# Performance work log

Hardware: AMD Instinct MI355X
Metric: run time of the kernel (lower is better)

The kernel has to match this reference:

```python
import jax, jax.numpy as jnp
import numpy as np

N, E, F = 50000, 1600000, 128
H1, C1 = 8, 16   # conv1: heads=8, out=16 -> concat 128
H2, C2 = 1, 16   # conv2: heads=1, out=num_classes=16


def _gat_conv(x, edge_index, W, a_src, a_dst, b, heads, out_ch):
    """PyG GATConv with self-loops, additive attention, dst-segmented softmax."""
    n = x.shape[0]
    loop = jnp.arange(n, dtype=edge_index.dtype)
    src = jnp.concatenate([edge_index[0], loop])  # [Et]
    dst = jnp.concatenate([edge_index[1], loop])  # [Et]
    h = (x @ W).reshape(n, heads, out_ch)                      # [N,H,C]
    alpha_s = jnp.sum(h * a_src[None], axis=-1)                # [N,H]
    alpha_d = jnp.sum(h * a_dst[None], axis=-1)                # [N,H]
    e = jax.nn.leaky_relu(alpha_s[src] + alpha_d[dst], 0.2)    # [Et,H]
    # segment softmax over destination node (self-loops guarantee nonempty segments)
    m = jax.lax.stop_gradient(jax.ops.segment_max(e, dst, num_segments=n))
    ex = jnp.exp(e - m[dst])
    denom = jax.ops.segment_sum(ex, dst, num_segments=n)
    alpha = ex / denom[dst]                                    # [Et,H]
    msg = h[src] * alpha[:, :, None]                           # [Et,H,C]
    out = jax.ops.segment_sum(msg, dst, num_segments=n)        # [N,H,C]
    return out.reshape(n, heads * out_ch) + b


def setup_inputs() -> dict:
    key = jax.random.key(0)
    ks = jax.random.split(key, 10)
    sc = 0.1
    x = jax.random.normal(ks[0], (N, F), dtype=jnp.float32)
    edge_index = jax.random.randint(ks[1], (2, E), 0, N, dtype=jnp.int32)
    return {
        "x": x,
        "edge_index": edge_index,
        "W1": jax.random.normal(ks[2], (F, H1 * C1), dtype=jnp.float32) * sc,
        "a_src1": jax.random.normal(ks[3], (H1, C1), dtype=jnp.float32) * sc,
        "a_dst1": jax.random.normal(ks[4], (H1, C1), dtype=jnp.float32) * sc,
        "b1": jnp.zeros((H1 * C1,), dtype=jnp.float32),
        "W2": jax.random.normal(ks[5], (H1 * C1, H2 * C2), dtype=jnp.float32) * sc,
        "a_src2": jax.random.normal(ks[6], (H2, C2), dtype=jnp.float32) * sc,
        "a_dst2": jax.random.normal(ks[7], (H2, C2), dtype=jnp.float32) * sc,
        "b2": jnp.zeros((H2 * C2,), dtype=jnp.float32),
    }


def reference(x, edge_index, W1, a_src1, a_dst1, b1, W2, a_src2, a_dst2, b2):
    h = _gat_conv(x, edge_index, W1, a_src1, a_dst1, b1, H1, C1)
    h = jax.nn.elu(h)
    # dropout p=0.6 is identity in eval mode
    return _gat_conv(h, edge_index, W2, a_src2, a_dst2, b2, H2, C2)
```

## Files before the change

kernel.cpp:

```cpp
#include <hip/hip_runtime.h>
#include <hip/hip_bf16.h>

#define NN 50000
#define NE 1600000
#define ET (NE + NN)
#define H1 8
#define C1 16
#define D1 128
#define C2 16
#define NB1 196
#define OCTW 6250
#define NSL 64
#define SLE (NE / NSL)

#define HIST_NB 512
#define PACK_NB 1563
#define SCAT_NB 512
#define GEMM_NB 782

typedef unsigned short u16;
typedef unsigned int u32;
typedef u32 u32x4 __attribute__((ext_vector_type(4)));

__device__ void hist_role(int hbid, char* smem, const int* __restrict__ ei,
                          u16* __restrict__ hs) {
  int* hl = (int*)smem;
  const int oct = hbid & 7;
  const int s   = hbid >> 3;
  const int lo  = oct * OCTW;
  const int tid = threadIdx.x;
  for (int j = tid; j < OCTW; j += 256) hl[j] = 0;
  __syncthreads();
  const int4* dp = (const int4*)(ei + NE) + (size_t)s * (SLE / 4);
  for (int g = tid; g < SLE / 4; g += 256) {
    int4 v = dp[g];
    int a = v.x - lo, b = v.y - lo, c = v.z - lo, d = v.w - lo;
    if ((unsigned)a < OCTW) atomicAdd(&hl[a], 1);
    if ((unsigned)b < OCTW) atomicAdd(&hl[b], 1);
    if ((unsigned)c < OCTW) atomicAdd(&hl[c], 1);
    if ((unsigned)d < OCTW) atomicAdd(&hl[d], 1);
  }
  __syncthreads();
  u16* out = hs + (size_t)s * NN + lo;
  for (int j = tid; j < OCTW; j += 256) out[j] = (u16)hl[j];
}

__device__ void pack_role(int pbid, const int* __restrict__ ei,
                          u16* __restrict__ src16, u16* __restrict__ dst16) {
  int i = pbid * 256 + threadIdx.x;
  if (i >= NE / 4) return;
  int4 s = ((const int4*)ei)[i];
  int4 d = ((const int4*)(ei + NE))[i];
  ushort4 sp; sp.x = (u16)s.x; sp.y = (u16)s.y; sp.z = (u16)s.z; sp.w = (u16)s.w;
  ushort4 dp; dp.x = (u16)d.x; dp.y = (u16)d.y; dp.z = (u16)d.z; dp.w = (u16)d.w;
  ((ushort4*)src16)[i] = sp;
  ((ushort4*)dst16)[i] = dp;
}

__global__ __launch_bounds__(256) void k1_fused(const int* __restrict__ ei,
    u16* __restrict__ hs, u16* __restrict__ src16, u16* __restrict__ dst16) {
  __shared__ __align__(16) char smem[25088];
  const int bid = blockIdx.x;
  if (bid < HIST_NB) hist_role(bid, smem, ei, hs);
  else pack_role(bid - HIST_NB, ei, src16, dst16);
}

__global__ __launch_bounds__(256) void scan1_k(u16* __restrict__ hs,
                                               int* __restrict__ deg32,
                                               int* __restrict__ incl,
                                               int* __restrict__ bsum) {
  __shared__ int sm[256];
  int t = threadIdx.x, i = blockIdx.x * 256 + t;
  int v = 0;
  if (i < NN) {
    int run = 0;
#pragma unroll
    for (int s = 0; s < NSL; ++s) {
      int c = (int)hs[(size_t)s * NN + i];
      hs[(size_t)s * NN + i] = (u16)run;
      run += c;
    }
    v = run + 1;
    deg32[i] = v;
  }
  sm[t] = v; __syncthreads();
  for (int off = 1; off < 256; off <<= 1) {
    int u = (t >= off) ? sm[t - off] : 0;
    __syncthreads();
    sm[t] += u;
    __syncthreads();
  }
  if (i < NN) incl[i] = sm[t];
  if (t == 255) bsum[blockIdx.x] = sm[255];
}

__global__ __launch_bounds__(256) void scan2_k(const int* __restrict__ bsum, int* __restrict__ boff) {
  __shared__ int sm[256];
  int t = threadIdx.x;
  int v = (t < NB1) ? bsum[t] : 0;
  sm[t] = v; __syncthreads();
  for (int off = 1; off < 256; off <<= 1) {
    int u = (t >= off) ? sm[t - off] : 0;
    __syncthreads();
    sm[t] += u;
    __syncthreads();
  }
  if (t < NB1) boff[t] = sm[t] - v;
}

__global__ __launch_bounds__(256) void scan3_k(const int* __restrict__ deg32,
                                               const int* __restrict__ incl,
                                               const int* __restrict__ boff,
                                               int* __restrict__ rowptr,
                                               u16* __restrict__ srcs) {
  int i = blockIdx.x * 256 + threadIdx.x;
  if (i >= NN) return;
  int dg = deg32[i];
  int r = incl[i] - dg + boff[i >> 8];
  rowptr[i] = r;
  srcs[r + dg - 1] = (u16)i;
  if (i == 0) rowptr[NN] = ET;
}

__device__ void scatter_role(int sbid, char* smem, const u16* __restrict__ src16,
    const u16* __restrict__ dst16, const int* __restrict__ rowptr,
    const u16* __restrict__ hs, u16* __restrict__ srcs) {
  int* cur = (int*)smem;
  const int oct = sbid & 7;
  const int s   = sbid >> 3;
  const int lo  = oct * OCTW;
  const int tid = threadIdx.x;
  const u16* seed = hs + (size_t)s * NN + lo;
  for (int j = tid; j < OCTW; j += 256)
    cur[j] = rowptr[lo + j] + (int)seed[j];
  __syncthreads();
  const u32x4* dp = (const u32x4*)dst16 + (size_t)s * (SLE / 8);
  const u32x4* sp = (const u32x4*)src16 + (size_t)s * (SLE / 8);
  for (int g = tid; g < SLE / 8; g += 256) {
    u32x4 dv = __builtin_nontemporal_load(&dp[g]);
    u32x4 sv = __builtin_nontemporal_load(&sp[g]);
#pragma unroll
    for (int q = 0; q < 4; ++q) {
      int d0 = (int)(dv[q] & 0xffffu) - lo;
      int d1 = (int)(dv[q] >> 16) - lo;
      if ((unsigned)d0 < OCTW) srcs[atomicAdd(&cur[d0], 1)] = (u16)(sv[q] & 0xffffu);
      if ((unsigned)d1 < OCTW) srcs[atomicAdd(&cur[d1], 1)] = (u16)(sv[q] >> 16);
    }
  }
}

__device__ void gemm1_role(int bid, char* smem, const float* __restrict__ X,
    const float* __restrict__ W, const float* __restrict__ aS,
    const float* __restrict__ aD, __hip_bfloat16* __restrict__ Yb,
    float* __restrict__ as1, float* __restrict__ ad1) {
  float (*Xs)[68]  = (float(*)[68])smem;
  float (*Wt)[128] = (float(*)[128])(smem + 8704);
  const int tid = threadIdx.x;
  const int tx = tid & 31;
  const int ty = tid >> 5;
  const int row0 = bid * 64;
  float acc[8][4] = {};

  for (int kt = 0; kt < D1; kt += 32) {
    {
      int r = tid >> 3, c4 = tid & 7;
#pragma unroll
      for (int it = 0; it < 2; ++it) {
        int row = r + it * 32;
        int grow = row0 + row; if (grow > NN - 1) grow = NN - 1;
        float4 v = *(const float4*)(X + (size_t)grow * D1 + kt + c4 * 4);
        Xs[c4 * 4 + 0][row] = v.x; Xs[c4 * 4 + 1][row] = v.y;
        Xs[c4 * 4 + 2][row] = v.z; Xs[c4 * 4 + 3][row] = v.w;
      }
    }
#pragma unroll
    for (int it = 0; it < 4; ++it) {
      int idx = it * 256 + tid;
      int kk = idx >> 5, cc = (idx & 31) * 4;
      *(float4*)&Wt[kk][cc] = *(const float4*)(W + (size_t)(kt + kk) * D1 + cc);
    }
    __syncthreads();
#pragma unroll
    for (int k = 0; k < 32; ++k) {
      float4 w4 = *(const float4*)&Wt[k][tx * 4];
      float4 xa = *(const float4*)&Xs[k][ty * 8];
      float4 xb = *(const float4*)&Xs[k][ty * 8 + 4];
      float xv[8] = {xa.x, xa.y, xa.z, xa.w, xb.x, xb.y, xb.z, xb.w};
      float wv[4] = {w4.x, w4.y, w4.z, w4.w};
#pragma unroll
      for (int rr = 0; rr < 8; ++rr)
#pragma unroll
        for (int cc = 0; cc < 4; ++cc)
          acc[rr][cc] = fmaf(xv[rr], wv[cc], acc[rr][cc]);
    }
    __syncthreads();
  }

  const int h = tx >> 2;
  const int cin = (tx * 4) & 15;
  float a_sv[4], a_dv[4];
#pragma unroll
  for (int j = 0; j < 4; ++j) { a_sv[j] = aS[h * 16 + cin + j]; a_dv[j] = aD[h * 16 + cin + j]; }
#pragma unroll
  for (int rr = 0; rr < 8; ++rr) {
    int grow = row0 + ty * 8 + rr;
    if (grow < NN) {
      union { ushort4 u; __hip_bfloat16 hh[4]; } pk;
      pk.hh[0] = __float2bfloat16(acc[rr][0]);
      pk.hh[1] = __float2bfloat16(acc[rr][1]);
      pk.hh[2] = __float2bfloat16(acc[rr][2]);
      pk.hh[3] = __float2bfloat16(acc[rr][3]);
      *(ushort4*)(Yb + (size_t)grow * D1 + tx * 4) = pk.u;
      float ps = acc[rr][0] * a_sv[0] + acc[rr][1] * a_sv[1] + acc[rr][2] * a_sv[2] + acc[rr][3] * a_sv[3];
      float pd = acc[rr][0] * a_dv[0] + acc[rr][1] * a_dv[1] + acc[rr][2] * a_dv[2] + acc[rr][3] * a_dv[3];
      ps += __shfl_xor(ps, 1); pd += __shfl_xor(pd, 1);
      ps += __shfl_xor(ps, 2); pd += __shfl_xor(pd, 2);
      if ((tx & 3) == 0) { as1[grow * H1 + h] = ps; ad1[grow * H1 + h] = pd; }
    }
  }
}

__global__ __launch_bounds__(256) void k2_fused(const u16* __restrict__ src16,
    const u16* __restrict__ dst16, const int* __restrict__ rowptr,
    const u16* __restrict__ hs, u16* __restrict__ srcs,
    const float* __restrict__ X, const float* __restrict__ W,
    const float* __restrict__ aS, const float* __restrict__ aD,
    __hip_bfloat16* __restrict__ Yb, float* __restrict__ as1, float* __restrict__ ad1) {
  __shared__ __align__(16) char smem[25088];
  const int bid = blockIdx.x;
  if (bid < SCAT_NB) scatter_role(bid, smem, src16, dst16, rowptr, hs, srcs);
  else gemm1_role(bid - SCAT_NB, smem, X, W, aS, aD, Yb, as1, ad1);
}

__global__ __launch_bounds__(128) void agg1_k(const int* __restrict__ rowptr,
    const u16* __restrict__ srcs, const u32* __restrict__ h1u,
    const float* __restrict__ as, const float* __restrict__ ad,
    const float* __restrict__ b, float* __restrict__ z) {
  __shared__ int ssrc[2][64];
  __shared__ float wl[2][64 * 9];
  __shared__ int lens[2];
  const int w = threadIdx.x >> 6;
  const int lane = threadIdx.x & 63;
  const int d = blockIdx.x * 2 + w;
  const int h = lane >> 3;
  const int beg = rowptr[d], end = rowptr[d + 1];
  if (lane == 0) lens[w] = end - beg;
  __syncthreads();
  const int nb = (max(lens[0], lens[1]) + 63) >> 6;
  const float4 adv0 = *(const float4*)(ad + (size_t)d * H1);
  const float4 adv1 = *(const float4*)(ad + (size_t)d * H1 + 4);
  float aL0 = 0, aL1 = 0, aL2 = 0, aL3 = 0;
  float aH0 = 0, aH1 = 0, aH2 = 0, aH3 = 0;
  float dn0 = 0, dn1 = 0, dn2 = 0, dn3 = 0;
  for (int it = 0; it < nb; ++it) {
    const int base = beg + (it << 6);
    int m = end - base; m = m < 0 ? 0 : (m > 64 ? 64 : m);
    if (lane < m) {
      int s = (int)srcs[base + lane];
      ssrc[w][lane] = s;
      const float4 a0 = *(const float4*)(as + (size_t)s * H1);
      const float4 a1 = *(const float4*)(as + (size_t)s * H1 + 4);
      float* wp = &wl[w][lane * 9];
      float e;
      e = a0.x + adv0.x; e = e > 0.f ? e : 0.2f * e; wp[0] = __expf(e);
      e = a0.y + adv0.y; e = e > 0.f ? e : 0.2f * e; wp[1] = __expf(e);
      e = a0.z + adv0.z; e = e > 0.f ? e : 0.2f * e; wp[2] = __expf(e);
      e = a0.w + adv0.w; e = e > 0.f ? e : 0.2f * e; wp[3] = __expf(e);
      e = a1.x + adv1.x; e = e > 0.f ? e : 0.2f * e; wp[4] = __expf(e);
      e = a1.y + adv1.y; e = e > 0.f ? e : 0.2f * e; wp[5] = __expf(e);
      e = a1.z + adv1.z; e = e > 0.f ? e : 0.2f * e; wp[6] = __expf(e);
      e = a1.w + adv1.w; e = e > 0.f ? e : 0.2f * e; wp[7] = __expf(e);
    }
    __syncthreads();
    int j = 0;
    for (; j + 4 <= m; j += 4) {
      int s0 = ssrc[w][j], s1 = ssrc[w][j + 1], s2 = ssrc[w][j + 2], s3 = ssrc[w][j + 3];
      float w0 = wl[w][(j + 0) * 9 + h], w1 = wl[w][(j + 1) * 9 + h];
      float w2 = wl[w][(j + 2) * 9 + h], w3 = wl[w][(j + 3) * 9 + h];
      u32 v0 = h1u[(size_t)s0 * 64 + lane];
      u32 v1 = h1u[(size_t)s1 * 64 + lane];
      u32 v2 = h1u[(size_t)s2 * 64 + lane];
      u32 v3 = h1u[(size_t)s3 * 64 + lane];
      dn0 += w0; dn1 += w1; dn2 += w2; dn3 += w3;
      aL0 = fmaf(w0, __uint_as_float(v0 << 16), aL0);
      aH0 = fmaf(w0, __uint_as_float(v0 & 0xffff0000u), aH0);
      aL1 = fmaf(w1, __uint_as_float(v1 << 16), aL1);
      aH1 = fmaf(w1, __uint_as_float(v1 & 0xffff0000u), aH1);
      aL2 = fmaf(w2, __uint_as_float(v2 << 16), aL2);
      aH2 = fmaf(w2, __uint_as_float(v2 & 0xffff0000u), aH2);
      aL3 = fmaf(w3, __uint_as_float(v3 << 16), aL3);
      aH3 = fmaf(w3, __uint_as_float(v3 & 0xffff0000u), aH3);
    }
    for (; j < m; ++j) {
      int s0 = ssrc[w][j];
      float w0 = wl[w][j * 9 + h];
      u32 v0 = h1u[(size_t)s0 * 64 + lane];
      dn0 += w0;
      aL0 = fmaf(w0, __uint_as_float(v0 << 16), aL0);
      aH0 = fmaf(w0, __uint_as_float(v0 & 0xffff0000u), aH0);
    }
    __syncthreads();
  }
  float den = (dn0 + dn1) + (dn2 + dn3);
  float aL = (aL0 + aL1) + (aL2 + aL3);
  float aH = (aH0 + aH1) + (aH2 + aH3);
  float inv = 1.f / den;
  float2 bb = *(const float2*)(b + lane * 2);
  float v0 = aL * inv + bb.x;
  float v1 = aH * inv + bb.y;
  v0 = v0 > 0.f ? v0 : __expf(v0) - 1.f;
  v1 = v1 > 0.f ? v1 : __expf(v1) - 1.f;
  float2 o = {v0, v1};
  *(float2*)(z + (size_t)d * D1 + lane * 2) = o;
}

__global__ __launch_bounds__(256) void gemm2_k(const float* __restrict__ Z,
    const float* __restrict__ W, const float* __restrict__ aS,
    const float* __restrict__ aD, __hip_bfloat16* __restrict__ Yb,
    float* __restrict__ as2, float* __restrict__ ad2) {
  __shared__ float Ws[D1][C2];
  __shared__ float Zs[16][D1 + 4];
  const int tid = threadIdx.x;
  for (int i = tid; i < D1 * C2; i += 256) Ws[i >> 4][i & 15] = W[i];
  const int rb = blockIdx.x * 16;
  {
    int r = tid >> 5, c4 = (tid & 31) * 4;
#pragma unroll
    for (int it = 0; it < 2; ++it) {
      int rr = r + it * 8;
      float4 v = *(const float4*)(Z + (size_t)(rb + rr) * D1 + c4);
      *(float4*)&Zs[rr][c4] = v;
    }
  }
  __syncthreads();
  const int r = tid >> 4, c = tid & 15;
  float a0 = 0, a1 = 0, a2 = 0, a3 = 0;
#pragma unroll
  for (int k = 0; k < D1; k += 4) {
    float4 z4 = *(const float4*)&Zs[r][k];
    a0 = fmaf(z4.x, Ws[k][c], a0);
    a1 = fmaf(z4.y, Ws[k + 1][c], a1);
    a2 = fmaf(z4.z, Ws[k + 2][c], a2);
    a3 = fmaf(z4.w, Ws[k + 3][c], a3);
  }
  float acc = (a0 + a1) + (a2 + a3);
  Yb[(size_t)(rb + r) * C2 + c] = __float2bfloat16(acc);
  float ps = acc * aS[c], pd = acc * aD[c];
  ps += __shfl_xor(ps, 1); pd += __shfl_xor(pd, 1);
  ps += __shfl_xor(ps, 2); pd += __shfl_xor(pd, 2);
  ps += __shfl_xor(ps, 4); pd += __shfl_xor(pd, 4);
  ps += __shfl_xor(ps, 8); pd += __shfl_xor(pd, 8);
  if (c == 0) { as2[rb + r] = ps; ad2[rb + r] = pd; }
}

__global__ __launch_bounds__(256) void agg2_k(const int* __restrict__ rowptr,
    const u16* __restrict__ srcs, const u32* __restrict__ h2u,
    const float* __restrict__ as, const float* __restrict__ ad,
    const float* __restrict__ b, float* __restrict__ outp) {
  const int wv = threadIdx.x >> 6;
  const int lane = threadIdx.x & 63;
  const int d = blockIdx.x * 4 + wv;
  const int j8 = lane >> 3, cp = lane & 7;
  const int beg = rowptr[d], end = rowptr[d + 1];
  const float adv = ad[d];
  float a0 = 0, a1 = 0, den = 0;
  for (int base = beg; base < end; base += 64) {
    const int m = end - base;
    float wreg = 0.f; int sreg = 0;
    if (lane < m) {
      sreg = (int)srcs[base + lane];
      float e = as[sreg] + adv;
      e = e > 0.f ? e : 0.2f * e;
      wreg = __expf(e);
    }
    const int mm = m < 64 ? m : 64;
    const int rounds = (mm + 7) >> 3;
    for (int r = 0; r < rounds; ++r) {
      int src_lane = r * 8 + j8;
      float wgt = __shfl(wreg, src_lane);
      int s     = __shfl(sreg, src_lane);
      if (wgt > 0.f) {
        u32 v = h2u[(size_t)s * 8 + cp];
        den += wgt;
        a0 = fmaf(wgt, __uint_as_float(v << 16), a0);
        a1 = fmaf(wgt, __uint_as_float(v & 0xffff0000u), a1);
      }
    }
  }
#pragma unroll
  for (int off = 8; off < 64; off <<= 1) {
    a0 += __shfl_xor(a0, off);
    a1 += __shfl_xor(a1, off);
    den += __shfl_xor(den, off);
  }
  if (j8 == 0) {
    float inv = 1.f / den;
    float2 bb = *(const float2*)(b + cp * 2);
    float2 o = {a0 * inv + bb.x, a1 * inv + bb.y};
    *(float2*)(outp + (size_t)d * C2 + cp * 2) = o;
  }
}

extern "C" void kernel_launch(void* const* d_in, const int* in_sizes, int n_in,
                              void* d_out, int out_size, void* d_ws, size_t ws_size,
                              hipStream_t stream) {
  const float* x    = (const float*)d_in[0];
  const int*   ei   = (const int*)d_in[1];
  const float* W1   = (const float*)d_in[2];
  const float* aS1  = (const float*)d_in[3];
  const float* aD1  = (const float*)d_in[4];
  const float* b1   = (const float*)d_in[5];
  const float* W2   = (const float*)d_in[6];
  const float* aS2  = (const float*)d_in[7];
  const float* aD2  = (const float*)d_in[8];
  const float* b2   = (const float*)d_in[9];
  float* outp = (float*)d_out;

  char* p = (char*)d_ws;
  __hip_bfloat16* h1b = (__hip_bfloat16*)p; p += (size_t)NN * D1 * 2;
  float* z    = (float*)p; p += (size_t)NN * D1 * 4;
  float* as1  = (float*)p; p += (size_t)NN * H1 * 4;
  float* ad1  = (float*)p; p += (size_t)NN * H1 * 4;
  u16*   hs     = (u16*)p; p += (size_t)NSL * NN * 2;
  int*   deg32  = (int*)p; p += (size_t)NN * 4;
  int*   incl   = (int*)p; p += (size_t)NN * 4;
  int*   rowptr = (int*)p; p += (size_t)(NN + 1) * 4;
  int*   bsum   = (int*)p; p += 256 * 4;
  int*   boff   = (int*)p; p += 256 * 4;
  u16*   srcs   = (u16*)p; p += (size_t)ET * 2;
  u16*   src16  = (u16*)p; p += (size_t)NE * 2;
  u16*   dst16  = (u16*)p; p += (size_t)NE * 2;
  __hip_bfloat16* h2b = h1b;
  float* as2 = (float*)(h1b + (size_t)NN * C2);
  float* ad2 = as2 + NN;

  k1_fused<<<HIST_NB + PACK_NB, 256, 0, stream>>>(ei, hs, src16, dst16);

  scan1_k<<<NB1, 256, 0, stream>>>(hs, deg32, incl, bsum);
  scan2_k<<<1, 256, 0, stream>>>(bsum, boff);
  scan3_k<<<NB1, 256, 0, stream>>>(deg32, incl, boff, rowptr, srcs);

  k2_fused<<<SCAT_NB + GEMM_NB, 256, 0, stream>>>(
      src16, dst16, rowptr, hs, srcs, x, W1, aS1, aD1, h1b, as1, ad1);

  agg1_k <<<NN / 2, 128, 0, stream>>>(rowptr, srcs, (const u32*)h1b, as1, ad1, b1, z);

  gemm2_k<<<NN / 16, 256, 0, stream>>>(z, W2, aS2, aD2, h2b, as2, ad2);
  agg2_k <<<NN / 4, 256, 0, stream>>>(rowptr, srcs, (const u32*)h2b, as2, ad2, b2, outp);
}
```

Baseline: 253.7 us.

## Use bf16 MFMA for layer-1 GEMM with folded attention weights, store z as bf16

Adds a small prep role that transposes W1 to bf16 and appends folded attention vectors W1·a_src and W1·a_dst as extra output columns. The layer-1 GEMM then runs on MFMA 16x16x32 bf16 instructions and produces the attention logits in the same pass. The fp32 scalar-FMA tiling and the separate reduction are removed. The layer-1 output z is also stored as bf16, which halves its write and read traffic in gemm2. The cost is lower precision in x, the folded attention logits and z, which could hurt accuracy.

```diff
diff --git a/kernel.cpp b/kernel.cpp
--- a/kernel.cpp
+++ b/kernel.cpp
@@ -15,12 +15,15 @@
 
 #define HIST_NB 512
 #define PACK_NB 1563
+#define PREP_NB 8
 #define SCAT_NB 512
 #define GEMM_NB 782
 
 typedef unsigned short u16;
 typedef unsigned int u32;
 typedef u32 u32x4 __attribute__((ext_vector_type(4)));
+typedef __bf16 bf16x8 __attribute__((ext_vector_type(8)));
+typedef float f32x4v __attribute__((ext_vector_type(4)));
 
 __device__ void hist_role(int hbid, char* smem, const int* __restrict__ ei,
                           u16* __restrict__ hs) {
@@ -57,12 +60,37 @@
   ((ushort4*)dst16)[i] = dp;
 }
 
+__device__ void prep_role(int pbid, const float* __restrict__ W1,
+    const float* __restrict__ aS, const float* __restrict__ aD,
+    __hip_bfloat16* __restrict__ WextT) {
+  const int k = threadIdx.x;
+  if (k >= 128) return;
+  const int h = pbid;
+#pragma unroll
+  for (int j = 0; j < 16; ++j) {
+    int n = h * 16 + j;
+    WextT[(size_t)n * 128 + k] = __float2bfloat16(W1[(size_t)k * 128 + n]);
+  }
+  float s = 0.f, dv = 0.f;
+#pragma unroll
+  for (int c = 0; c < 16; ++c) {
+    float w = W1[(size_t)k * 128 + h * 16 + c];
+    s  = fmaf(w, aS[h * 16 + c], s);
+    dv = fmaf(w, aD[h * 16 + c], dv);
+  }
+  WextT[(size_t)(128 + h) * 128 + k] = __float2bfloat16(s);
+  WextT[(size_t)(136 + h) * 128 + k] = __float2bfloat16(dv);
+}
+
 __global__ __launch_bounds__(256) void k1_fused(const int* __restrict__ ei,
-    u16* __restrict__ hs, u16* __restrict__ src16, u16* __restrict__ dst16) {
+    u16* __restrict__ hs, u16* __restrict__ src16, u16* __restrict__ dst16,
+    const float* __restrict__ W1, const float* __restrict__ aS,
+    const float* __restrict__ aD, __hip_bfloat16* __restrict__ WextT) {
   __shared__ __align__(16) char smem[25088];
   const int bid = blockIdx.x;
   if (bid < HIST_NB) hist_role(bid, smem, ei, hs);
-  else pack_role(bid - HIST_NB, ei, src16, dst16);
+  else if (bid < HIST_NB + PACK_NB) pack_role(bid - HIST_NB, ei, src16, dst16);
+  else prep_role(bid - HIST_NB - PACK_NB, W1, aS, aD, WextT);
 }
 
 __global__ __launch_bounds__(256) void scan1_k(u16* __restrict__ hs,
@@ -149,73 +177,43 @@
   }
 }
 
-__device__ void gemm1_role(int bid, char* smem, const float* __restrict__ X,
-    const float* __restrict__ W, const float* __restrict__ aS,
-    const float* __restrict__ aD, __hip_bfloat16* __restrict__ Yb,
-    float* __restrict__ as1, float* __restrict__ ad1) {
-  float (*Xs)[68]  = (float(*)[68])smem;
-  float (*Wt)[128] = (float(*)[128])(smem + 8704);
+__device__ void gemm1_role(int bid, const float* __restrict__ X,
+    const __hip_bfloat16* __restrict__ WextT,
+    __hip_bfloat16* __restrict__ Yb, float* __restrict__ as1, float* __restrict__ ad1) {
   const int tid = threadIdx.x;
-  const int tx = tid & 31;
-  const int ty = tid >> 5;
-  const int row0 = bid * 64;
-  float acc[8][4] = {};
-
-  for (int kt = 0; kt < D1; kt += 32) {
-    {
-      int r = tid >> 3, c4 = tid & 7;
-#pragma unroll
-      for (int it = 0; it < 2; ++it) {
-        int row = r + it * 32;
-        int grow = row0 + row; if (grow > NN - 1) grow = NN - 1;
-        float4 v = *(const float4*)(X + (size_t)grow * D1 + kt + c4 * 4);
-        Xs[c4 * 4 + 0][row] = v.x; Xs[c4 * 4 + 1][row] = v.y;
-        Xs[c4 * 4 + 2][row] = v.z; Xs[c4 * 4 + 3][row] = v.w;
-      }
-    }
-#pragma unroll
-    for (int it = 0; it < 4; ++it) {
-      int idx = it * 256 + tid;
-      int kk = idx >> 5, cc = (idx & 31) * 4;
-      *(float4*)&Wt[kk][cc] = *(const float4*)(W + (size_t)(kt + kk) * D1 + cc);
-    }
-    __syncthreads();
-#pragma unroll
-    for (int k = 0; k < 32; ++k) {
-      float4 w4 = *(const float4*)&Wt[k][tx * 4];
-      float4 xa = *(const float4*)&Xs[k][ty * 8];
-      float4 xb = *(const float4*)&Xs[k][ty * 8 + 4];
-      float xv[8] = {xa.x, xa.y, xa.z, xa.w, xb.x, xb.y, xb.z, xb.w};
-      float wv[4] = {w4.x, w4.y, w4.z, w4.w};
-#pragma unroll
-      for (int rr = 0; rr < 8; ++rr)
-#pragma unroll
-        for (int cc = 0; cc < 4; ++cc)
-          acc[rr][cc] = fmaf(xv[rr], wv[cc], acc[rr][cc]);
-    }
-    __syncthreads();
-  }
-
-  const int h = tx >> 2;
-  const int cin = (tx * 4) & 15;
-  float a_sv[4], a_dv[4];
-#pragma unroll
-  for (int j = 0; j < 4; ++j) { a_sv[j] = aS[h * 16 + cin + j]; a_dv[j] = aD[h * 16 + cin + j]; }
-#pragma unroll
-  for (int rr = 0; rr < 8; ++rr) {
-    int grow = row0 + ty * 8 + rr;
-    if (grow < NN) {
-      union { ushort4 u; __hip_bfloat16 hh[4]; } pk;
-      pk.hh[0] = __float2bfloat16(acc[rr][0]);
-      pk.hh[1] = __float2bfloat16(acc[rr][1]);
-      pk.hh[2] = __float2bfloat16(acc[rr][2]);
-      pk.hh[3] = __float2bfloat16(acc[rr][3]);
-      *(ushort4*)(Yb + (size_t)grow * D1 + tx * 4) = pk.u;
-      float ps = acc[rr][0] * a_sv[0] + acc[rr][1] * a_sv[1] + acc[rr][2] * a_sv[2] + acc[rr][3] * a_sv[3];
-      float pd = acc[rr][0] * a_dv[0] + acc[rr][1] * a_dv[1] + acc[rr][2] * a_dv[2] + acc[rr][3] * a_dv[3];
-      ps += __shfl_xor(ps, 1); pd += __shfl_xor(pd, 1);
-      ps += __shfl_xor(ps, 2); pd += __shfl_xor(pd, 2);
-      if ((tx & 3) == 0) { as1[grow * H1 + h] = ps; ad1[grow * H1 + h] = pd; }
+  const int wv = tid >> 6, lane = tid & 63;
+  const int row0 = bid * 64 + wv * 16;
+  const int mrow = lane & 15;
+  const int kq = lane >> 4;
+  int garow = row0 + mrow; if (garow > NN - 1) garow = NN - 1;
+  const float* xrow = X + (size_t)garow * D1 + kq * 8;
+  const char* bbase = (const char*)WextT + (size_t)mrow * 256 + kq * 16;
+  f32x4v acc[9] = {};
+#pragma unroll
+  for (int kt = 0; kt < 4; ++kt) {
+    float4 xa = *(const float4*)(xrow + kt * 32);
+    float4 xb = *(const float4*)(xrow + kt * 32 + 4);
+    bf16x8 af;
+    af[0] = (__bf16)xa.x; af[1] = (__bf16)xa.y; af[2] = (__bf16)xa.z; af[3] = (__bf16)xa.w;
+    af[4] = (__bf16)xb.x; af[5] = (__bf16)xb.y; af[6] = (__bf16)xb.z; af[7] = (__bf16)xb.w;
+#pragma unroll
+    for (int nt = 0; nt < 9; ++nt) {
+      u32x4 braw = *(const u32x4*)(bbase + (size_t)nt * 4096 + kt * 64);
+      bf16x8 bfr = __builtin_bit_cast(bf16x8, braw);
+      acc[nt] = __builtin_amdgcn_mfma_f32_16x16x32_bf16(af, bfr, acc[nt], 0, 0, 0);
+    }
+  }
+  const int cl = lane & 15;
+#pragma unroll
+  for (int reg = 0; reg < 4; ++reg) {
+    int gr = row0 + (lane >> 4) * 4 + reg;
+    if (gr < NN) {
+#pragma unroll
+      for (int nt = 0; nt < 8; ++nt)
+        Yb[(size_t)gr * D1 + nt * 16 + cl] = __float2bfloat16(acc[nt][reg]);
+      float lv = acc[8][reg];
+      if (cl < 8) as1[gr * H1 + cl] = lv;
+      else        ad1[gr * H1 + (cl - 8)] = lv;
     }
   }
 }
@@ -223,19 +221,18 @@
 __global__ __launch_bounds__(256) void k2_fused(const u16* __restrict__ src16,
     const u16* __restrict__ dst16, const int* __restrict__ rowptr,
     const u16* __restrict__ hs, u16* __restrict__ srcs,
-    const float* __restrict__ X, const float* __restrict__ W,
-    const float* __restrict__ aS, const float* __restrict__ aD,
+    const float* __restrict__ X, const __hip_bfloat16* __restrict__ WextT,
     __hip_bfloat16* __restrict__ Yb, float* __restrict__ as1, float* __restrict__ ad1) {
   __shared__ __align__(16) char smem[25088];
   const int bid = blockIdx.x;
   if (bid < SCAT_NB) scatter_role(bid, smem, src16, dst16, rowptr, hs, srcs);
-  else gemm1_role(bid - SCAT_NB, smem, X, W, aS, aD, Yb, as1, ad1);
+  else gemm1_role(bid - SCAT_NB, X, WextT, Yb, as1, ad1);
 }
 
 __global__ __launch_bounds__(128) void agg1_k(const int* __restrict__ rowptr,
     const u16* __restrict__ srcs, const u32* __restrict__ h1u,
     const float* __restrict__ as, const float* __restrict__ ad,
-    const float* __restrict__ b, float* __restrict__ z) {
+    const float* __restrict__ b, u32* __restrict__ zb) {
   __shared__ int ssrc[2][64];
   __shared__ float wl[2][64 * 9];
   __shared__ int lens[2];
@@ -310,11 +307,12 @@
   float v1 = aH * inv + bb.y;
   v0 = v0 > 0.f ? v0 : __expf(v0) - 1.f;
   v1 = v1 > 0.f ? v1 : __expf(v1) - 1.f;
-  float2 o = {v0, v1};
-  *(float2*)(z + (size_t)d * D1 + lane * 2) = o;
-}
-
-__global__ __launch_bounds__(256) void gemm2_k(const float* __restrict__ Z,
+  __hip_bfloat16 z0 = __float2bfloat16(v0), z1 = __float2bfloat16(v1);
+  u32 pu = ((u32)(*(u16*)&z1) << 16) | (u32)(*(u16*)&z0);
+  zb[(size_t)d * 64 + lane] = pu;
+}
+
+__global__ __launch_bounds__(256) void gemm2_k(const u32* __restrict__ Zb,
     const float* __restrict__ W, const float* __restrict__ aS,
     const float* __restrict__ aD, __hip_bfloat16* __restrict__ Yb,
     float* __restrict__ as2, float* __restrict__ ad2) {
@@ -324,12 +322,13 @@
   for (int i = tid; i < D1 * C2; i += 256) Ws[i >> 4][i & 15] = W[i];
   const int rb = blockIdx.x * 16;
   {
-    int r = tid >> 5, c4 = (tid & 31) * 4;
-#pragma unroll
-    for (int it = 0; it < 2; ++it) {
-      int rr = r + it * 8;
-      float4 v = *(const float4*)(Z + (size_t)(rb + rr) * D1 + c4);
-      *(float4*)&Zs[rr][c4] = v;
+    int r = tid >> 4, c8 = tid & 15;
+    u32x4 raw = *(const u32x4*)(Zb + (size_t)(rb + r) * 64 + c8 * 4);
+    float* dst = &Zs[r][c8 * 8];
+#pragma unroll
+    for (int q = 0; q < 4; ++q) {
+      dst[2 * q]     = __uint_as_float(raw[q] << 16);
+      dst[2 * q + 1] = __uint_as_float(raw[q] & 0xffff0000u);
     }
   }
   __syncthreads();
@@ -418,9 +417,10 @@
 
   char* p = (char*)d_ws;
   __hip_bfloat16* h1b = (__hip_bfloat16*)p; p += (size_t)NN * D1 * 2;
-  float* z    = (float*)p; p += (size_t)NN * D1 * 4;
+  u32* zb   = (u32*)p; p += (size_t)NN * 64 * 4;
   float* as1  = (float*)p; p += (size_t)NN * H1 * 4;
   float* ad1  = (float*)p; p += (size_t)NN * H1 * 4;
+  __hip_bfloat16* WextT = (__hip_bfloat16*)p; p += (size_t)144 * 128 * 2;
   u16*   hs     = (u16*)p; p += (size_t)NSL * NN * 2;
   int*   deg32  = (int*)p; p += (size_t)NN * 4;
   int*   incl   = (int*)p; p += (size_t)NN * 4;
@@ -434,17 +434,18 @@
   float* as2 = (float*)(h1b + (size_t)NN * C2);
   float* ad2 = as2 + NN;
 
-  k1_fused<<<HIST_NB + PACK_NB, 256, 0, stream>>>(ei, hs, src16, dst16);
+  k1_fused<<<HIST_NB + PACK_NB + PREP_NB, 256, 0, stream>>>(
+      ei, hs, src16, dst16, W1, aS1, aD1, WextT);
 
   scan1_k<<<NB1, 256, 0, stream>>>(hs, deg32, incl, bsum);
   scan2_k<<<1, 256, 0, stream>>>(bsum, boff);
   scan3_k<<<NB1, 256, 0, stream>>>(deg32, incl, boff, rowptr, srcs);
 
   k2_fused<<<SCAT_NB + GEMM_NB, 256, 0, stream>>>(
-      src16, dst16, rowptr, hs, srcs, x, W1, aS1, aD1, h1b, as1, ad1);
-
-  agg1_k <<<NN / 2, 128, 0, stream>>>(rowptr, srcs, (const u32*)h1b, as1, ad1, b1, z);
-
-  gemm2_k<<<NN / 16, 256, 0, stream>>>(z, W2, aS2, aD2, h2b, as2, ad2);
+      src16, dst16, rowptr, hs, srcs, x, WextT, h1b, as1, ad1);
+
+  agg1_k <<<NN / 2, 128, 0, stream>>>(rowptr, srcs, (const u32*)h1b, as1, ad1, b1, zb);
+
+  gemm2_k<<<NN / 16, 256, 0, stream>>>(zb, W2, aS2, aD2, h2b, as2, ad2);
   agg2_k <<<NN / 4, 256, 0, stream>>>(rowptr, srcs, (const u32*)h2b, as2, ad2, b2, outp);
 }
```

Measured after the change: 255.4 us. No clear change (+0.7%).
